# Kernel tuning notes

Hardware: AMD Instinct MI355X
Metric: run time of the kernel (lower is better)

Reference implementation:

```python
import jax, jax.numpy as jnp
import numpy as np

D = 1024
F = 256
EPS = 1e-5


def layer_norm(x, g, b):
    mu = jnp.mean(x, axis=-1, keepdims=True)
    var = jnp.mean((x - mu) ** 2, axis=-1, keepdims=True)
    return (x - mu) * jax.lax.rsqrt(var + EPS) * g + b


def setup_inputs() -> dict:
    key = jax.random.key(0)
    ks = jax.random.split(key, 8)
    B, S = 4, 4096
    return {
        "bottom_up_input": jax.random.normal(ks[0], (B, S, D), dtype=jnp.float32),
        "top_down_prediction": jax.random.normal(ks[1], (B, S, D), dtype=jnp.float32),
        "W_spec": jax.random.normal(ks[2], (2 * F, D), dtype=jnp.float32) * 0.02,
        "log_decay": jnp.linspace(-3.0, -0.001, F, dtype=jnp.float32),
        "frequencies": jax.random.normal(ks[3], (F,), dtype=jnp.float32) * 0.1,
        "W_from": jax.random.normal(ks[4], (D, 2 * F), dtype=jnp.float32) * 0.02,
        "ln1_g": jnp.ones((D,), jnp.float32),
        "ln1_b": jnp.zeros((D,), jnp.float32),
        "W1": jax.random.normal(ks[5], (D, D), dtype=jnp.float32) * 0.02,
        "b1": jnp.zeros((D,), jnp.float32),
        "W2": jax.random.normal(ks[6], (D, D), dtype=jnp.float32) * 0.02,
        "b2": jnp.zeros((D,), jnp.float32),
        "ln2_g": jnp.ones((D,), jnp.float32),
        "ln2_b": jnp.zeros((D,), jnp.float32),
        "error_weight": jnp.asarray(0.1, jnp.float32),
    }


def spectral_conv(x, W_spec, log_decay, frequencies, W_from, ln1_g, ln1_b):
    # x: [B,S,D]
    x = layer_norm(x, ln1_g, ln1_b)
    B, S, _ = x.shape
    spectral = jnp.einsum('bsd,fd->bsf', x, W_spec)  # [B,S,2F]
    u = jax.lax.complex(spectral[..., :F], spectral[..., F:])  # [B,S,F] complex
    decay = jax.nn.sigmoid(log_decay)
    omega = jnp.tanh(frequencies) * 0.1  # dt = 1.0
    rot = jax.lax.complex(jnp.cos(omega), jnp.sin(omega))  # [F]
    A = (decay * rot).astype(jnp.complex64)  # [F]
    # kernel[t] = A^t * rot, built with cumprod as in the original
    ones = jnp.ones((1, F), dtype=A.dtype)
    A_seq = jnp.broadcast_to(A[None, :], (S - 1, F))
    powers = jnp.cumprod(jnp.concatenate([ones, A_seq], axis=0), axis=0)  # [S,F]
    kernel = (powers * rot[None, :])[None]  # [1,S,F]
    n_fft = 2 * S
    U_f = jnp.fft.fft(u, n=n_fft, axis=1)
    K_f = jnp.fft.fft(kernel, n=n_fft, axis=1)
    y = jnp.fft.ifft(U_f * K_f, n=n_fft, axis=1)[:, :S, :]  # [B,S,F]
    spectral_out = jnp.concatenate([y.real, y.imag], axis=-1)  # [B,S,2F]
    return jnp.einsum('bsf,df->bsd', spectral_out, W_from)


def reference(bottom_up_input, top_down_prediction, W_spec, log_decay, frequencies,
              W_from, ln1_g, ln1_b, W1, b1, W2, b2, ln2_g, ln2_b, error_weight):
    bu_repr = spectral_conv(bottom_up_input, W_spec, log_decay, frequencies,
                            W_from, ln1_g, ln1_b)
    error = jnp.clip(bu_repr - top_down_prediction, -1.0, 1.0)
    corrected = bu_repr - jax.nn.sigmoid(error_weight) * error
    prediction_error = jnp.clip(jnp.mean(error ** 2), 0.0, 1.0)
    h = jax.nn.gelu(jnp.einsum('bsd,ed->bse', corrected, W1) + b1, approximate=False)
    h = jnp.einsum('bsd,ed->bse', h, W2) + b2
    next_prediction = layer_norm(h, ln2_g, ln2_b)
    return corrected, next_prediction, prediction_error
```

## Files before the change

kernel.cpp:

```cpp
#include <hip/hip_runtime.h>
#include <math.h>

#define Dn 1024
#define Fn 256
#define Sn 4096
#define Bn 4
#define Mn (Bn*Sn)
#define CHn 256
#define NCn (Sn/CHn)

typedef __bf16 bf16x8 __attribute__((ext_vector_type(8)));
typedef float  f32x4  __attribute__((ext_vector_type(4)));

__device__ inline unsigned short f2bf(float f) {
  unsigned int u = __float_as_uint(f);
  u += 0x7fffu + ((u >> 16) & 1u);
  return (unsigned short)(u >> 16);
}

__device__ inline void async16(const void* g, void* l) {
  __builtin_amdgcn_global_load_lds(
      (__attribute__((address_space(1))) void*)(g),
      (__attribute__((address_space(3))) void*)(l), 16, 0, 0);
}

__global__ __launch_bounds__(256) void convert_weights(
    const float* __restrict__ wspec, const float* __restrict__ wfrom,
    const float* __restrict__ w1, const float* __restrict__ w2,
    unsigned short* __restrict__ o_spec, unsigned short* __restrict__ o_from,
    unsigned short* __restrict__ o_w1, unsigned short* __restrict__ o_w2) {
  int i = blockIdx.x * 256 + threadIdx.x;
  if (i < 524288) {
    o_spec[i] = f2bf(wspec[i]);
    o_from[i] = f2bf(wfrom[i]);
  }
  o_w1[i] = f2bf(w1[i]);
  o_w2[i] = f2bf(w2[i]);
}

template <int OUT_BF16>
__global__ __launch_bounds__(256) void ln_kernel(
    const float* __restrict__ x, const float* __restrict__ g,
    const float* __restrict__ b, void* __restrict__ out) {
  int row = blockIdx.x, tid = threadIdx.x;
  int wid = tid >> 6, lane = tid & 63;
  float4 v = ((const float4*)(x + (size_t)row * Dn))[tid];
  float s  = v.x + v.y + v.z + v.w;
  float ss = v.x * v.x + v.y * v.y + v.z * v.z + v.w * v.w;
  #pragma unroll
  for (int o = 32; o; o >>= 1) {
    s  += __shfl_down(s, o);
    ss += __shfl_down(ss, o);
  }
  __shared__ float r1[4], r2[4];
  if (lane == 0) { r1[wid] = s; r2[wid] = ss; }
  __syncthreads();
  s  = r1[0] + r1[1] + r1[2] + r1[3];
  ss = r2[0] + r2[1] + r2[2] + r2[3];
  float mu  = s * (1.0f / Dn);
  float var = ss * (1.0f / Dn) - mu * mu;
  float rs  = rsqrtf(var + 1e-5f);
  float4 gv = ((const float4*)g)[tid];
  float4 bv = ((const float4*)b)[tid];
  float o0 = (v.x - mu) * rs * gv.x + bv.x;
  float o1 = (v.y - mu) * rs * gv.y + bv.y;
  float o2 = (v.z - mu) * rs * gv.z + bv.z;
  float o3 = (v.w - mu) * rs * gv.w + bv.w;
  if (OUT_BF16) {
    ushort4 w;
    w.x = f2bf(o0); w.y = f2bf(o1); w.z = f2bf(o2); w.w = f2bf(o3);
    ((ushort4*)out)[(size_t)row * 256 + tid] = w;
  } else {
    float4 w; w.x = o0; w.y = o1; w.z = o2; w.w = o3;
    ((float4*)out)[(size_t)row * 256 + tid] = w;
  }
}

template <int MODE>
__global__ __launch_bounds__(256) void gemm_bt(
    const unsigned short* __restrict__ A, const unsigned short* __restrict__ Bw,
    int K, int N,
    float* __restrict__ outF, unsigned short* __restrict__ outH,
    const float* __restrict__ td, const float* __restrict__ bias,
    const float* __restrict__ ew, float* __restrict__ errAcc) {
  __shared__ unsigned short As[128 * 32];
  __shared__ unsigned short Bs[128 * 32];
  __shared__ float red[4];

  int tid = threadIdx.x;
  int wid = tid >> 6, lane = tid & 63;
  int wm = wid >> 1, wn = wid & 1;
  int quad = lane >> 4, l16 = lane & 15;
  int bm = blockIdx.y, bn = blockIdx.x;

  int r_lo = lane >> 2;
  int c8   = (lane & 3) * 8;

  const unsigned short* Abase = A + (size_t)bm * 128 * K;
  const unsigned short* Bbase = Bw + (size_t)bn * 128 * K;

  f32x4 acc[4][4] = {};

  for (int k0 = 0; k0 < K; k0 += 32) {
    #pragma unroll
    for (int s = 0; s < 2; ++s) {
      int chunk = s * 4 + wid;
      int r = chunk * 16 + r_lo;
      async16(Abase + (size_t)r * K + k0 + c8, As + chunk * 512);
      async16(Bbase + (size_t)r * K + k0 + c8, Bs + chunk * 512);
    }
    __syncthreads();
    bf16x8 af[4], bf[4];
    #pragma unroll
    for (int i = 0; i < 4; i++)
      af[i] = *(const bf16x8*)(As + (wm * 64 + i * 16 + l16) * 32 + quad * 8);
    #pragma unroll
    for (int j = 0; j < 4; j++)
      bf[j] = *(const bf16x8*)(Bs + (wn * 64 + j * 16 + l16) * 32 + quad * 8);
    #pragma unroll
    for (int i = 0; i < 4; i++)
      #pragma unroll
      for (int j = 0; j < 4; j++)
        acc[i][j] = __builtin_amdgcn_mfma_f32_16x16x32_bf16(af[i], bf[j], acc[i][j], 0, 0, 0);
    __syncthreads();
  }

  float esum = 0.0f;
  float sigw = 0.0f;
  if (MODE == 1) sigw = 1.0f / (1.0f + expf(-ew[0]));

  #pragma unroll
  for (int i = 0; i < 4; i++) {
    int row_base = bm * 128 + wm * 64 + i * 16 + quad * 4;
    #pragma unroll
    for (int j = 0; j < 4; j++) {
      int col = bn * 128 + wn * 64 + j * 16 + l16;
      #pragma unroll
      for (int r = 0; r < 4; r++) {
        size_t idx = (size_t)(row_base + r) * N + col;
        float v = acc[i][j][r];
        if (MODE == 0) {
          outF[idx] = v;
        } else if (MODE == 1) {
          float e = v - td[idx];
          e = fminf(fmaxf(e, -1.0f), 1.0f);
          float corr = v - sigw * e;
          outF[idx] = corr;
          outH[idx] = f2bf(corr);
          esum += e * e;
        } else if (MODE == 2) {
          float h = v + bias[col];
          float gel = 0.5f * h * (1.0f + erff(h * 0.70710678118654752f));
          outH[idx] = f2bf(gel);
        } else {
          outF[idx] = v + bias[col];
        }
      }
    }
  }

  if (MODE == 1) {
    #pragma unroll
    for (int o = 32; o; o >>= 1) esum += __shfl_down(esum, o);
    if (lane == 0) red[wid] = esum;
    __syncthreads();
    if (tid == 0) atomicAdd(errAcc, red[0] + red[1] + red[2] + red[3]);
  }
}

__global__ __launch_bounds__(256) void scan_partial(
    const float* __restrict__ spec, const float* __restrict__ log_decay,
    const float* __restrict__ freq, float2* __restrict__ chunkfin) {
  int f = threadIdx.x;
  int bx = blockIdx.x;
  int b = bx / NCn, c = bx % NCn;
  float dec = 1.0f / (1.0f + expf(-log_decay[f]));
  float om  = tanhf(freq[f]) * 0.1f;
  float Are = dec * cosf(om), Aim = dec * sinf(om);
  const float* u = spec + ((size_t)b * Sn + (size_t)c * CHn) * 512 + f;
  float sre = 0.0f, sim = 0.0f;
  for (int t = 0; t < CHn; t++) {
    float ure = u[(size_t)t * 512];
    float uim = u[(size_t)t * 512 + 256];
    float nre = Are * sre - Aim * sim + ure;
    float nim = Are * sim + Aim * sre + uim;
    sre = nre; sim = nim;
  }
  chunkfin[(size_t)bx * 256 + f] = make_float2(sre, sim);
}

__global__ __launch_bounds__(256) void scan_carry(
    const float* __restrict__ log_decay, const float* __restrict__ freq,
    const float2* __restrict__ chunkfin, float2* __restrict__ carries) {
  int f = threadIdx.x;
  int b = blockIdx.x;
  float dec = 1.0f / (1.0f + expf(-log_decay[f]));
  float om  = tanhf(freq[f]) * 0.1f;
  float pre = dec * cosf(om), pim = dec * sinf(om);
  #pragma unroll
  for (int i = 0; i < 8; i++) {
    float nr = pre * pre - pim * pim;
    float ni = 2.0f * pre * pim;
    pre = nr; pim = ni;
  }
  float sre = 0.0f, sim = 0.0f;
  for (int c = 0; c < NCn; c++) {
    carries[(size_t)(b * NCn + c) * 256 + f] = make_float2(sre, sim);
    float2 cf = chunkfin[(size_t)(b * NCn + c) * 256 + f];
    float nre = pre * sre - pim * sim + cf.x;
    float nim = pre * sim + pim * sre + cf.y;
    sre = nre; sim = nim;
  }
}

__global__ __launch_bounds__(256) void scan_final(
    const float* __restrict__ spec, const float* __restrict__ log_decay,
    const float* __restrict__ freq, const float2* __restrict__ carries,
    unsigned short* __restrict__ outH) {
  int f = threadIdx.x;
  int bx = blockIdx.x;
  int b = bx / NCn, c = bx % NCn;
  float dec = 1.0f / (1.0f + expf(-log_decay[f]));
  float om  = tanhf(freq[f]) * 0.1f;
  float Are = dec * cosf(om), Aim = dec * sinf(om);
  float Rre = cosf(om), Rim = sinf(om);
  float2 s0 = carries[(size_t)bx * 256 + f];
  float sre = s0.x, sim = s0.y;
  const float* u = spec + ((size_t)b * Sn + (size_t)c * CHn) * 512 + f;
  unsigned short* o = outH + ((size_t)b * Sn + (size_t)c * CHn) * 512 + f;
  for (int t = 0; t < CHn; t++) {
    float ure = u[(size_t)t * 512];
    float uim = u[(size_t)t * 512 + 256];
    float nre = Are * sre - Aim * sim + ure;
    float nim = Are * sim + Aim * sre + uim;
    sre = nre; sim = nim;
    o[(size_t)t * 512]       = f2bf(Rre * sre - Rim * sim);
    o[(size_t)t * 512 + 256] = f2bf(Rre * sim + Rim * sre);
  }
}

__global__ void finalize_err(const float* __restrict__ errAcc, float* __restrict__ out) {
  float m = errAcc[0] * (1.0f / 16777216.0f);
  out[0] = fminf(fmaxf(m, 0.0f), 1.0f);
}

extern "C" void kernel_launch(void* const* d_in, const int* in_sizes, int n_in,
                              void* d_out, int out_size, void* d_ws, size_t ws_size,
                              hipStream_t stream) {
  (void)in_sizes; (void)n_in; (void)out_size; (void)ws_size;
  const float* x     = (const float*)d_in[0];
  const float* td    = (const float*)d_in[1];
  const float* wspec = (const float*)d_in[2];
  const float* logd  = (const float*)d_in[3];
  const float* freq  = (const float*)d_in[4];
  const float* wfrom = (const float*)d_in[5];
  const float* g1    = (const float*)d_in[6];
  const float* b1ln  = (const float*)d_in[7];
  const float* W1    = (const float*)d_in[8];
  const float* b1    = (const float*)d_in[9];
  const float* W2    = (const float*)d_in[10];
  const float* b2    = (const float*)d_in[11];
  const float* g2    = (const float*)d_in[12];
  const float* b2ln  = (const float*)d_in[13];
  const float* ew    = (const float*)d_in[14];

  char* ws = (char*)d_ws;
  size_t off = 0;
  float* errAcc = (float*)(ws + off);              off += 256;
  unsigned short* wspec_h = (unsigned short*)(ws + off); off += (size_t)512 * 1024 * 2;
  unsigned short* wfrom_h = (unsigned short*)(ws + off); off += (size_t)1024 * 512 * 2;
  unsigned short* w1_h    = (unsigned short*)(ws + off); off += (size_t)1024 * 1024 * 2;
  unsigned short* w2_h    = (unsigned short*)(ws + off); off += (size_t)1024 * 1024 * 2;
  unsigned short* xn_h   = (unsigned short*)(ws + off);
  unsigned short* corr_h = (unsigned short*)(ws + off); off += (size_t)Mn * 1024 * 2;
  float* spec          = (float*)(ws + off);
  unsigned short* h1_h = (unsigned short*)(ws + off);  off += (size_t)Mn * 512 * 4;
  unsigned short* so_h = (unsigned short*)(ws + off);  off += (size_t)Mn * 512 * 2;
  float2* chunkfin = (float2*)(ws + off);              off += (size_t)Bn * NCn * 256 * 8;
  float2* carries  = (float2*)(ws + off);              off += (size_t)Bn * NCn * 256 * 8;

  float* outCorr = (float*)d_out;
  float* outNP   = outCorr + (size_t)Mn * 1024;
  float* outErr  = outNP + (size_t)Mn * 1024;

  hipMemsetAsync(errAcc, 0, 4, stream);
  convert_weights<<<4096, 256, 0, stream>>>(wspec, wfrom, W1, W2,
                                            wspec_h, wfrom_h, w1_h, w2_h);
  ln_kernel<1><<<Mn, 256, 0, stream>>>(x, g1, b1ln, xn_h);
  gemm_bt<0><<<dim3(512 / 128, Mn / 128), 256, 0, stream>>>(
      xn_h, wspec_h, 1024, 512, spec, nullptr, nullptr, nullptr, nullptr, nullptr);
  scan_partial<<<Bn * NCn, 256, 0, stream>>>(spec, logd, freq, chunkfin);
  scan_carry<<<Bn, 256, 0, stream>>>(logd, freq, chunkfin, carries);
  scan_final<<<Bn * NCn, 256, 0, stream>>>(spec, logd, freq, carries, so_h);
  gemm_bt<1><<<dim3(1024 / 128, Mn / 128), 256, 0, stream>>>(
      so_h, wfrom_h, 512, 1024, outCorr, corr_h, td, nullptr, ew, errAcc);
  gemm_bt<2><<<dim3(1024 / 128, Mn / 128), 256, 0, stream>>>(
      corr_h, w1_h, 1024, 1024, nullptr, h1_h, nullptr, b1, nullptr, nullptr);
  gemm_bt<3><<<dim3(1024 / 128, Mn / 128), 256, 0, stream>>>(
      h1_h, w2_h, 1024, 1024, outNP, nullptr, nullptr, b2, nullptr, nullptr);
  ln_kernel<0><<<Mn, 256, 0, stream>>>(outNP, g2, b2ln, outNP);
  finalize_err<<<1, 1, 0, stream>>>(errAcc, outErr);
}
```

Measured before the change: 538.4 us.

## Triple-buffer GEMM LDS loads, group-swizzle tiles, store spectral projection as bf16

The GEMM main loop now uses three LDS stages, issuing async global-to-LDS loads two tiles ahead with explicit vmcnt waits and a single barrier per k-step instead of two. Block indices are remapped in groups of eight rows for better L2 reuse. The spectral projection output is written as bf16 instead of fp32, so the scan kernels read half the bytes. This costs more LDS per block and adds bf16 rounding on the scan input.

Result: faster. 512.4 us (-4.8%).

```diff
diff --git a/kernel.cpp b/kernel.cpp
--- a/kernel.cpp
+++ b/kernel.cpp
@@ -17,12 +17,18 @@
   u += 0x7fffu + ((u >> 16) & 1u);
   return (unsigned short)(u >> 16);
 }
+__device__ inline float bf2f(unsigned short s) {
+  return __uint_as_float(((unsigned int)s) << 16);
+}
 
 __device__ inline void async16(const void* g, void* l) {
   __builtin_amdgcn_global_load_lds(
       (__attribute__((address_space(1))) void*)(g),
       (__attribute__((address_space(3))) void*)(l), 16, 0, 0);
 }
+
+#define WAITVM(n) __builtin_amdgcn_s_waitcnt(0xF70 | (n))
+#define BARRIER() asm volatile("s_barrier" ::: "memory")
 
 __global__ __launch_bounds__(256) void convert_weights(
     const float* __restrict__ wspec, const float* __restrict__ wfrom,
@@ -83,15 +89,20 @@
     float* __restrict__ outF, unsigned short* __restrict__ outH,
     const float* __restrict__ td, const float* __restrict__ bias,
     const float* __restrict__ ew, float* __restrict__ errAcc) {
-  __shared__ unsigned short As[128 * 32];
-  __shared__ unsigned short Bs[128 * 32];
+  __shared__ unsigned short As[3 * 4096];
+  __shared__ unsigned short Bs[3 * 4096];
   __shared__ float red[4];
 
   int tid = threadIdx.x;
   int wid = tid >> 6, lane = tid & 63;
   int wm = wid >> 1, wn = wid & 1;
   int quad = lane >> 4, l16 = lane & 15;
-  int bm = blockIdx.y, bn = blockIdx.x;
+
+  int g = blockIdx.x + gridDim.x * blockIdx.y;
+  int nbn = gridDim.x;
+  int gh = g >> 3;
+  int bn = gh % nbn;
+  int bm = (g & 7) + (gh / nbn) * 8;
 
   int r_lo = lane >> 2;
   int c8   = (lane & 3) * 8;
@@ -101,28 +112,44 @@
 
   f32x4 acc[4][4] = {};
 
-  for (int k0 = 0; k0 < K; k0 += 32) {
+  const int T = K >> 5;
+  auto issue = [&](int t, int stg) {
+    int k0 = t << 5;
     #pragma unroll
     for (int s = 0; s < 2; ++s) {
       int chunk = s * 4 + wid;
       int r = chunk * 16 + r_lo;
-      async16(Abase + (size_t)r * K + k0 + c8, As + chunk * 512);
-      async16(Bbase + (size_t)r * K + k0 + c8, Bs + chunk * 512);
+      async16(Abase + (size_t)r * K + k0 + c8, As + stg * 4096 + chunk * 512);
+      async16(Bbase + (size_t)r * K + k0 + c8, Bs + stg * 4096 + chunk * 512);
     }
-    __syncthreads();
+  };
+
+  issue(0, 0);
+  if (T > 1) issue(1, 1);
+
+  int stg = 0, stg2 = 2;
+  for (int k = 0; k < T; ++k) {
+    if (k + 1 < T) WAITVM(4); else WAITVM(0);
+    BARRIER();
+    if (k + 2 < T) issue(k + 2, stg2);
+
+    const unsigned short* Ab = As + stg * 4096;
+    const unsigned short* Bb = Bs + stg * 4096;
     bf16x8 af[4], bf[4];
     #pragma unroll
     for (int i = 0; i < 4; i++)
-      af[i] = *(const bf16x8*)(As + (wm * 64 + i * 16 + l16) * 32 + quad * 8);
+      af[i] = *(const bf16x8*)(Ab + (wm * 64 + i * 16 + l16) * 32 + quad * 8);
     #pragma unroll
     for (int j = 0; j < 4; j++)
-      bf[j] = *(const bf16x8*)(Bs + (wn * 64 + j * 16 + l16) * 32 + quad * 8);
+      bf[j] = *(const bf16x8*)(Bb + (wn * 64 + j * 16 + l16) * 32 + quad * 8);
     #pragma unroll
     for (int i = 0; i < 4; i++)
       #pragma unroll
       for (int j = 0; j < 4; j++)
         acc[i][j] = __builtin_amdgcn_mfma_f32_16x16x32_bf16(af[i], bf[j], acc[i][j], 0, 0, 0);
-    __syncthreads();
+
+    stg  = (stg  == 2) ? 0 : stg  + 1;
+    stg2 = (stg2 == 2) ? 0 : stg2 + 1;
   }
 
   float esum = 0.0f;
@@ -140,7 +167,7 @@
         size_t idx = (size_t)(row_base + r) * N + col;
         float v = acc[i][j][r];
         if (MODE == 0) {
-          outF[idx] = v;
+          outH[idx] = f2bf(v);
         } else if (MODE == 1) {
           float e = v - td[idx];
           e = fminf(fmaxf(e, -1.0f), 1.0f);
@@ -169,7 +196,7 @@
 }
 
 __global__ __launch_bounds__(256) void scan_partial(
-    const float* __restrict__ spec, const float* __restrict__ log_decay,
+    const unsigned short* __restrict__ spec, const float* __restrict__ log_decay,
     const float* __restrict__ freq, float2* __restrict__ chunkfin) {
   int f = threadIdx.x;
   int bx = blockIdx.x;
@@ -177,11 +204,11 @@
   float dec = 1.0f / (1.0f + expf(-log_decay[f]));
   float om  = tanhf(freq[f]) * 0.1f;
   float Are = dec * cosf(om), Aim = dec * sinf(om);
-  const float* u = spec + ((size_t)b * Sn + (size_t)c * CHn) * 512 + f;
+  const unsigned short* u = spec + ((size_t)b * Sn + (size_t)c * CHn) * 512 + f;
   float sre = 0.0f, sim = 0.0f;
   for (int t = 0; t < CHn; t++) {
-    float ure = u[(size_t)t * 512];
-    float uim = u[(size_t)t * 512 + 256];
+    float ure = bf2f(u[(size_t)t * 512]);
+    float uim = bf2f(u[(size_t)t * 512 + 256]);
     float nre = Are * sre - Aim * sim + ure;
     float nim = Are * sim + Aim * sre + uim;
     sre = nre; sim = nim;
@@ -214,7 +241,7 @@
 }
 
 __global__ __launch_bounds__(256) void scan_final(
-    const float* __restrict__ spec, const float* __restrict__ log_decay,
+    const unsigned short* __restrict__ spec, const float* __restrict__ log_decay,
     const float* __restrict__ freq, const float2* __restrict__ carries,
     unsigned short* __restrict__ outH) {
   int f = threadIdx.x;
@@ -226,11 +253,11 @@
   float Rre = cosf(om), Rim = sinf(om);
   float2 s0 = carries[(size_t)bx * 256 + f];
   float sre = s0.x, sim = s0.y;
-  const float* u = spec + ((size_t)b * Sn + (size_t)c * CHn) * 512 + f;
+  const unsigned short* u = spec + ((size_t)b * Sn + (size_t)c * CHn) * 512 + f;
   unsigned short* o = outH + ((size_t)b * Sn + (size_t)c * CHn) * 512 + f;
   for (int t = 0; t < CHn; t++) {
-    float ure = u[(size_t)t * 512];
-    float uim = u[(size_t)t * 512 + 256];
+    float ure = bf2f(u[(size_t)t * 512]);
+    float uim = bf2f(u[(size_t)t * 512 + 256]);
     float nre = Are * sre - Aim * sim + ure;
     float nim = Are * sim + Aim * sre + uim;
     sre = nre; sim = nim;
@@ -273,8 +300,8 @@
   unsigned short* w2_h    = (unsigned short*)(ws + off); off += (size_t)1024 * 1024 * 2;
   unsigned short* xn_h   = (unsigned short*)(ws + off);
   unsigned short* corr_h = (unsigned short*)(ws + off); off += (size_t)Mn * 1024 * 2;
-  float* spec          = (float*)(ws + off);
-  unsigned short* h1_h = (unsigned short*)(ws + off);  off += (size_t)Mn * 512 * 4;
+  unsigned short* spec  = (unsigned short*)(ws + off);
+  unsigned short* h1_h  = (unsigned short*)(ws + off);  off += (size_t)Mn * 1024 * 2;
   unsigned short* so_h = (unsigned short*)(ws + off);  off += (size_t)Mn * 512 * 2;
   float2* chunkfin = (float2*)(ws + off);              off += (size_t)Bn * NCn * 256 * 8;
   float2* carries  = (float2*)(ws + off);              off += (size_t)Bn * NCn * 256 * 8;
@@ -288,7 +315,7 @@
                                             wspec_h, wfrom_h, w1_h, w2_h);
   ln_kernel<1><<<Mn, 256, 0, stream>>>(x, g1, b1ln, xn_h);
   gemm_bt<0><<<dim3(512 / 128, Mn / 128), 256, 0, stream>>>(
-      xn_h, wspec_h, 1024, 512, spec, nullptr, nullptr, nullptr, nullptr, nullptr);
+      xn_h, wspec_h, 1024, 512, nullptr, spec, nullptr, nullptr, nullptr, nullptr);
   scan_partial<<<Bn * NCn, 256, 0, stream>>>(spec, logd, freq, chunkfin);
   scan_carry<<<Bn, 256, 0, stream>>>(logd, freq, chunkfin, carries);
   scan_final<<<Bn * NCn, 256, 0, stream>>>(spec, logd, freq, carries, so_h);
```
